# Optimization experiments

Measured on AMD Instinct MI355X. Metric: run time of the kernel, lower is better.

## Reference

```python
import jax, jax.numpy as jnp
import numpy as np

N, ID, OD, M, S, L = 65536, 16, 8, 1024, 8, 64


def setup_inputs() -> dict:
    key = jax.random.key(0)
    k1, k2, k3, k4, k5, k6 = jax.random.split(key, 6)
    return {
        "x": jax.random.normal(k1, (N, ID), dtype=jnp.float32),
        "inducing_locations": jax.random.uniform(k2, (M, ID), dtype=jnp.float32),
        "inducing_weights": jax.random.normal(k3, (S, OD, M), dtype=jnp.float32),
        "prior_frequency": jax.random.normal(k4, (OD, ID, L), dtype=jnp.float32),
        "prior_phase": jax.random.uniform(k5, (OD, L), dtype=jnp.float32, maxval=2 * np.pi),
        "prior_weights": jax.random.normal(k6, (S, OD, L), dtype=jnp.float32),
    }


def _rbf_matrix(x, z):
    # ExponentiatedQuadratic with amplitude=1, length_scale=1:
    # k(x,z) = exp(-0.5 * ||x - z||^2)
    x2 = jnp.sum(x * x, axis=-1)[:, None]          # [N,1]
    z2 = jnp.sum(z * z, axis=-1)[None, :]          # [1,M]
    sq = jnp.maximum(x2 + z2 - 2.0 * (x @ z.T), 0.0)
    return jnp.exp(-0.5 * sq)                      # [N,M]


def reference(x, inducing_locations, inducing_weights, prior_frequency, prior_phase, prior_weights):
    # ---- prior (random Fourier features) ----
    # spectral_weights for unit RBF: outer_weights = ones((OD,L)), inner_weights = ones((ID,))
    # rescaled_x = x / 1 = x
    # basis_fn_inner_prod: [OD, N, L]
    inner = jnp.einsum('ni,oil->onl', x, prior_frequency)
    basis_fn = jnp.cos(inner + prior_phase[:, None, :])              # [OD,N,L]
    basis_weight = jnp.sqrt(2.0 / prior_frequency.shape[-1]) * prior_weights  # [S,OD,L]
    f_prior = jnp.einsum('onl,sol->son', basis_fn, basis_weight)     # [S,OD,N]

    # ---- data term (kernel matrix + matvec) ----
    K = _rbf_matrix(x, inducing_locations)                           # [N,M]
    f_data = jnp.einsum('nm,som->son', K, inducing_weights)          # [S,OD,N]

    return f_prior + f_data
```

## Files before the change

kernel.cpp:

```cpp
#include <hip/hip_runtime.h>
#include <hip/hip_bf16.h>

#define N_PTS 65536
#define LOG2E 1.4426950408889634f
#define INV2PI 0.15915494309189535f

typedef __attribute__((ext_vector_type(8))) short short8;
typedef __attribute__((ext_vector_type(4))) short short4v;
typedef __attribute__((ext_vector_type(4))) float float4v;
typedef __attribute__((ext_vector_type(4))) unsigned int uint4v;

#if __has_builtin(__builtin_amdgcn_exp2f)
#define EXP2F(x) __builtin_amdgcn_exp2f(x)
#else
#define EXP2F(x) exp2f(x)
#endif

#if __has_builtin(__builtin_amdgcn_cosf) && __has_builtin(__builtin_amdgcn_fractf)
#define COSR(x) __builtin_amdgcn_cosf(__builtin_amdgcn_fractf(x))
#else
#define COSR(x) __cosf((x) * 6.283185307179586f)
#endif

__device__ __forceinline__ short f2b(float f) {
    __hip_bfloat16 h = __float2bfloat16(f);
    return *(short*)&h;
}
__device__ __forceinline__ float b2f(short s) {
    __hip_bfloat16 h = *(__hip_bfloat16*)&s;
    return __bfloat162float(h);
}

__device__ __forceinline__ unsigned int pkbf(float a, float b) {
    unsigned int ua = __builtin_bit_cast(unsigned int, a) + 0x8000u;
    unsigned int ub = __builtin_bit_cast(unsigned int, b) + 0x8000u;
    return (ua >> 16) | (ub & 0xFFFF0000u);
}

#if __has_builtin(__builtin_amdgcn_mfma_f32_16x16x16bf16_1k)
#define HAVE_MFMA16 1
typedef short4v pafrag;
__device__ __forceinline__ float4v pmfma(pafrag a, pafrag b, float4v c) {
    return __builtin_amdgcn_mfma_f32_16x16x16bf16_1k(a, b, c, 0, 0, 0);
}
#else
#define HAVE_MFMA16 0
typedef short8 pafrag;
__device__ __forceinline__ float4v pmfma(pafrag a, pafrag b, float4v c) {
    return __builtin_amdgcn_mfma_f32_16x16x32_bf16(a, b, c, 0, 0, 0);
}
#endif

__device__ __forceinline__ pafrag ldrow(const short* base, int row16, int q, int c) {
#if HAVE_MFMA16
    return *(const pafrag*)(base + (size_t)(row16 + c) * 16 + 4 * q);
#else
    pafrag v = (pafrag)0;
    if (q < 2) v = *(const pafrag*)(base + (size_t)(row16 + c) * 16 + 8 * q);
    return v;
#endif
}
__device__ __forceinline__ pafrag mkxfrag(const float* x, size_t row, int q) {
#if HAVE_MFMA16
    float4v v = *(const float4v*)(x + row * 16 + 4 * q);
    pafrag a;
    a[0] = f2b(v.x); a[1] = f2b(v.y); a[2] = f2b(v.z); a[3] = f2b(v.w);
    return a;
#else
    pafrag a = (pafrag)0;
    if (q < 2) {
        const float4v* xp = (const float4v*)(x + row * 16 + 8 * q);
        float4v v0 = xp[0], v1 = xp[1];
        a[0] = f2b(v0.x); a[1] = f2b(v0.y); a[2] = f2b(v0.z); a[3] = f2b(v0.w);
        a[4] = f2b(v1.x); a[5] = f2b(v1.y); a[6] = f2b(v1.z); a[7] = f2b(v1.w);
    }
    return a;
#endif
}

__device__ __forceinline__ int permrow(int p) {
    return ((p & 12) << 1) + (p & 3) + ((p >> 4) << 2);
}

__global__ __launch_bounds__(256) void prep_kernel(
    const float* __restrict__ z, const float* __restrict__ W,
    const float* __restrict__ F, const float* __restrict__ pw,
    const float* __restrict__ ph,
    short* __restrict__ zb, short* __restrict__ FbB,
    short* __restrict__ BWd, short* __restrict__ Wtb,
    float* __restrict__ nz2P, float* __restrict__ phP)
{
    int t = blockIdx.x * 256 + threadIdx.x;
    if (t < 16384) {
        int row = t >> 4, i = t & 15;
        int src = (row & ~31) + permrow(row & 31);
        zb[t] = f2b(LOG2E * z[src * 16 + i]);
    } else if (t < 17408) {
        int m = t - 16384;
        int src = (m & ~31) + permrow(m & 31);
        const float4v* zp = (const float4v*)(z + (size_t)src * 16);
        float s = 0.f;
        #pragma unroll
        for (int k = 0; k < 4; k++) {
            float4v v = zp[k];
            float a0 = b2f(f2b(v.x)), a1 = b2f(f2b(v.y));
            float a2 = b2f(f2b(v.z)), a3 = b2f(f2b(v.w));
            s += a0 * a0 + a1 * a1 + a2 * a2 + a3 * a3;
        }
        nz2P[m] = -(0.5f * LOG2E * s);
    } else if (t < 25600) {
        int p = t - 17408;
        int row = p >> 4, i = p & 15;
        int srow = (row & ~31) + permrow(row & 31);
        int o = srow >> 6, l = srow & 63;
        FbB[p] = f2b(INV2PI * F[o * 1024 + i * 64 + l]);
    } else if (t < 58368) {
        int p = t - 25600;
        int so = p >> 9, ol = p & 511, o = ol >> 6;
        float v = ((so & 7) == o) ? 0.17677669529663687f * pw[so * 64 + (ol & 63)] : 0.f;
        BWd[p] = f2b(v);
    } else if (t < 123904) {
        int p = t - 58368;
        Wtb[p] = f2b(W[p]);
    } else {
        int j = t - 123904;
        int sj = (j & ~31) + permrow(j & 31);
        phP[j] = INV2PI * ph[sj];
    }
}

__global__ __launch_bounds__(256, 4) void fused_kernel(
    const float* __restrict__ x,
    const short* __restrict__ zb, const short* __restrict__ FbB,
    const short* __restrict__ BWd, const short* __restrict__ Wtb,
    const float* __restrict__ nz2P, const float* __restrict__ phP,
    float* __restrict__ out)
{
    __shared__ float x2c[64];
    __shared__ __align__(16) float rbufA[64 * 68];
    __shared__ __align__(16) float rbufB[64 * 68];

    const int tid = threadIdx.x;
    const int lane = tid & 63, w = tid >> 6;
    const int q = lane >> 4, c = lane & 15;
    const int n0 = blockIdx.x * 64;

    if (tid < 64) {
        float s = 0.f;
        const float4v* xr = (const float4v*)(x + (size_t)(n0 + tid) * 16);
        #pragma unroll
        for (int k = 0; k < 4; k++) {
            float4v v = xr[k];
            float a0 = b2f(f2b(v.x)), a1 = b2f(f2b(v.y));
            float a2 = b2f(f2b(v.z)), a3 = b2f(f2b(v.w));
            s += a0 * a0 + a1 * a1 + a2 * a2 + a3 * a3;
        }
        x2c[tid] = 0.5f * LOG2E * s;
    }

    pafrag ax[4];
    #pragma unroll
    for (int nt = 0; nt < 4; nt++)
        ax[nt] = mkxfrag(x, (size_t)(n0 + nt * 16 + c), q);

    float4v acc[4][4];
    #pragma unroll
    for (int a = 0; a < 4; a++)
        #pragma unroll
        for (int nt = 0; nt < 4; nt++) acc[a][nt] = (float4v)(0.f);

    __syncthreads();

    const int mbase = w * 256;
    #pragma unroll 2
    for (int mb = 0; mb < 8; mb++) {
        const int m0 = mbase + mb * 32;
        pafrag bzA = ldrow(zb, m0, q, c);
        pafrag bzB = ldrow(zb, m0 + 16, q, c);
        float4v c0A = *(const float4v*)(nz2P + m0 + 4 * q);
        float4v c0B = *(const float4v*)(nz2P + m0 + 16 + 4 * q);
        short8 aw0 = *(const short8*)(Wtb + (size_t)(0 * 16 + c) * 1024 + m0 + q * 8);
        short8 aw1 = *(const short8*)(Wtb + (size_t)(1 * 16 + c) * 1024 + m0 + q * 8);
        short8 aw2 = *(const short8*)(Wtb + (size_t)(2 * 16 + c) * 1024 + m0 + q * 8);
        short8 aw3 = *(const short8*)(Wtb + (size_t)(3 * 16 + c) * 1024 + m0 + q * 8);
        #pragma unroll
        for (int nt = 0; nt < 4; nt++) {
            float4v dA = pmfma(bzA, ax[nt], c0A);
            float4v dB = pmfma(bzB, ax[nt], c0B);
            uint4v u;
            u[0] = pkbf(EXP2F(dA[0]), EXP2F(dA[1]));
            u[1] = pkbf(EXP2F(dA[2]), EXP2F(dA[3]));
            u[2] = pkbf(EXP2F(dB[0]), EXP2F(dB[1]));
            u[3] = pkbf(EXP2F(dB[2]), EXP2F(dB[3]));
            short8 pb = __builtin_bit_cast(short8, u);
            acc[0][nt] = __builtin_amdgcn_mfma_f32_16x16x32_bf16(aw0, pb, acc[0][nt], 0, 0, 0);
            acc[1][nt] = __builtin_amdgcn_mfma_f32_16x16x32_bf16(aw1, pb, acc[1][nt], 0, 0, 0);
            acc[2][nt] = __builtin_amdgcn_mfma_f32_16x16x32_bf16(aw2, pb, acc[2][nt], 0, 0, 0);
            acc[3][nt] = __builtin_amdgcn_mfma_f32_16x16x32_bf16(aw3, pb, acc[3][nt], 0, 0, 0);
        }
    }

    #pragma unroll
    for (int nt = 0; nt < 4; nt++) {
        float sxv = EXP2F(-x2c[nt * 16 + c]);
        #pragma unroll
        for (int a = 0; a < 4; a++) acc[a][nt] *= sxv;
    }

    const int lbase = w * 128;
    #pragma unroll 2
    for (int lb = 0; lb < 4; lb++) {
        const int l0 = lbase + lb * 32;
        pafrag bfA = ldrow(FbB, l0, q, c);
        pafrag bfB = ldrow(FbB, l0 + 16, q, c);
        float4v c0A = *(const float4v*)(phP + l0 + 4 * q);
        float4v c0B = *(const float4v*)(phP + l0 + 16 + 4 * q);
        short8 aw0 = *(const short8*)(BWd + (size_t)(0 * 16 + c) * 512 + l0 + q * 8);
        short8 aw1 = *(const short8*)(BWd + (size_t)(1 * 16 + c) * 512 + l0 + q * 8);
        short8 aw2 = *(const short8*)(BWd + (size_t)(2 * 16 + c) * 512 + l0 + q * 8);
        short8 aw3 = *(const short8*)(BWd + (size_t)(3 * 16 + c) * 512 + l0 + q * 8);
        #pragma unroll
        for (int nt = 0; nt < 4; nt++) {
            float4v dA = pmfma(bfA, ax[nt], c0A);
            float4v dB = pmfma(bfB, ax[nt], c0B);
            uint4v u;
            u[0] = pkbf(COSR(dA[0]), COSR(dA[1]));
            u[1] = pkbf(COSR(dA[2]), COSR(dA[3]));
            u[2] = pkbf(COSR(dB[0]), COSR(dB[1]));
            u[3] = pkbf(COSR(dB[2]), COSR(dB[3]));
            short8 pb = __builtin_bit_cast(short8, u);
            acc[0][nt] = __builtin_amdgcn_mfma_f32_16x16x32_bf16(aw0, pb, acc[0][nt], 0, 0, 0);
            acc[1][nt] = __builtin_amdgcn_mfma_f32_16x16x32_bf16(aw1, pb, acc[1][nt], 0, 0, 0);
            acc[2][nt] = __builtin_amdgcn_mfma_f32_16x16x32_bf16(aw2, pb, acc[2][nt], 0, 0, 0);
            acc[3][nt] = __builtin_amdgcn_mfma_f32_16x16x32_bf16(aw3, pb, acc[3][nt], 0, 0, 0);
        }
    }

    __syncthreads();
    if (w & 1) {
        float* rb = (w == 1) ? rbufA : rbufB;
        #pragma unroll
        for (int a = 0; a < 4; a++)
            #pragma unroll
            for (int nt = 0; nt < 4; nt++)
                #pragma unroll
                for (int r = 0; r < 4; r++)
                    rb[(a * 16 + 4 * q + r) * 68 + nt * 16 + c] = acc[a][nt][r];
    }
    __syncthreads();
    if (!(w & 1)) {
        float* rb = (w == 0) ? rbufA : rbufB;
        #pragma unroll
        for (int a = 0; a < 4; a++)
            #pragma unroll
            for (int nt = 0; nt < 4; nt++)
                #pragma unroll
                for (int r = 0; r < 4; r++) {
                    int idx = (a * 16 + 4 * q + r) * 68 + nt * 16 + c;
                    rb[idx] += acc[a][nt][r];
                }
    }
    __syncthreads();
    #pragma unroll
    for (int k = 0; k < 16; k++) {
        int idx = k * 256 + tid;
        int row = idx >> 6, nn = idx & 63;
        out[(size_t)row * N_PTS + n0 + nn] = rbufA[row * 68 + nn] + rbufB[row * 68 + nn];
    }
}

extern "C" void kernel_launch(void* const* d_in, const int* in_sizes, int n_in,
                              void* d_out, int out_size, void* d_ws, size_t ws_size,
                              hipStream_t stream) {
    const float* x  = (const float*)d_in[0];
    const float* z  = (const float*)d_in[1];
    const float* W  = (const float*)d_in[2];
    const float* F  = (const float*)d_in[3];
    const float* ph = (const float*)d_in[4];
    const float* pw = (const float*)d_in[5];
    float* out = (float*)d_out;

    char* ws = (char*)d_ws;
    short* zb   = (short*)(ws);
    short* FbB  = (short*)(ws + 32768);
    short* BWd  = (short*)(ws + 49152);
    short* Wtb  = (short*)(ws + 114688);
    float* nz2P = (float*)(ws + 245760);
    float* phP  = (float*)(ws + 249856);

    prep_kernel<<<486, 256, 0, stream>>>(z, W, F, pw, ph, zb, FbB, BWd, Wtb, nz2P, phP);
    fused_kernel<<<1024, 256, 0, stream>>>(x, zb, FbB, BWd, Wtb, nz2P, phP, out);
}
```

Measured before the change: 107.6 us.

## Fold parameter prep kernel into fused kernel, converting to bf16 on the fly

Removes the separate prep kernel launch and workspace. The fused kernel now reads the fp32 inducing locations, weights, frequencies and prior weights directly and converts them to bf16 fragments inside the main loops. The per-inducing-point norms and the phases are computed per block into shared memory that reuses the reduction buffer. This trades one launch and a small global round trip for redundant conversion work and twice the fp32 global/L2 read traffic in every one of 1024 blocks, plus strided loads for the frequency fragments.

```diff
diff --git a/kernel.cpp b/kernel.cpp
--- a/kernel.cpp
+++ b/kernel.cpp
@@ -4,11 +4,13 @@
 #define N_PTS 65536
 #define LOG2E 1.4426950408889634f
 #define INV2PI 0.15915494309189535f
+#define PWSC 0.17677669529663687f
 
 typedef __attribute__((ext_vector_type(8))) short short8;
 typedef __attribute__((ext_vector_type(4))) short short4v;
 typedef __attribute__((ext_vector_type(4))) float float4v;
 typedef __attribute__((ext_vector_type(4))) unsigned int uint4v;
+typedef __attribute__((ext_vector_type(2))) unsigned int uint2v;
 
 #if __has_builtin(__builtin_amdgcn_exp2f)
 #define EXP2F(x) __builtin_amdgcn_exp2f(x)
@@ -51,15 +53,79 @@
 }
 #endif
 
-__device__ __forceinline__ pafrag ldrow(const short* base, int row16, int q, int c) {
+__device__ __forceinline__ int permrow(int p) {
+    return ((p & 12) << 1) + (p & 3) + ((p >> 4) << 2);
+}
+
+
+__device__ __forceinline__ pafrag mkzfrag(const float* __restrict__ z, int p, int q) {
+    int src = (p & ~31) + permrow(p & 31);
 #if HAVE_MFMA16
-    return *(const pafrag*)(base + (size_t)(row16 + c) * 16 + 4 * q);
-#else
-    pafrag v = (pafrag)0;
-    if (q < 2) v = *(const pafrag*)(base + (size_t)(row16 + c) * 16 + 8 * q);
-    return v;
-#endif
-}
+    float4v v = *(const float4v*)(z + (size_t)src * 16 + 4 * q);
+    uint2v u;
+    u[0] = pkbf(LOG2E * v.x, LOG2E * v.y);
+    u[1] = pkbf(LOG2E * v.z, LOG2E * v.w);
+    return __builtin_bit_cast(short4v, u);
+#else
+    pafrag a = (pafrag)0;
+    if (q < 2) {
+        const float4v* zp = (const float4v*)(z + (size_t)src * 16 + 8 * q);
+        float4v v0 = zp[0], v1 = zp[1];
+        uint4v u;
+        u[0] = pkbf(LOG2E * v0.x, LOG2E * v0.y);
+        u[1] = pkbf(LOG2E * v0.z, LOG2E * v0.w);
+        u[2] = pkbf(LOG2E * v1.x, LOG2E * v1.y);
+        u[3] = pkbf(LOG2E * v1.z, LOG2E * v1.w);
+        a = __builtin_bit_cast(short8, u);
+    }
+    return a;
+#endif
+}
+
+__device__ __forceinline__ pafrag mkffrag(const float* __restrict__ F, int p, int q) {
+    int srow = (p & ~31) + permrow(p & 31);
+    const float* fb = F + ((srow >> 6) << 10) + (srow & 63);
+#if HAVE_MFMA16
+    float d0 = fb[(4 * q + 0) * 64], d1 = fb[(4 * q + 1) * 64];
+    float d2 = fb[(4 * q + 2) * 64], d3 = fb[(4 * q + 3) * 64];
+    uint2v u;
+    u[0] = pkbf(INV2PI * d0, INV2PI * d1);
+    u[1] = pkbf(INV2PI * d2, INV2PI * d3);
+    return __builtin_bit_cast(short4v, u);
+#else
+    pafrag a = (pafrag)0;
+    if (q < 2) {
+        uint4v u;
+        #pragma unroll
+        for (int j = 0; j < 4; j++) {
+            float g0 = fb[(8 * q + 2 * j) * 64], g1 = fb[(8 * q + 2 * j + 1) * 64];
+            u[j] = pkbf(INV2PI * g0, INV2PI * g1);
+        }
+        a = __builtin_bit_cast(short8, u);
+    }
+    return a;
+#endif
+}
+
+__device__ __forceinline__ short8 mkwfrag(const float* __restrict__ W, int so, int base) {
+    const float4v* wp = (const float4v*)(W + (size_t)so * 1024 + base);
+    float4v v0 = wp[0], v1 = wp[1];
+    uint4v u;
+    u[0] = pkbf(v0.x, v0.y); u[1] = pkbf(v0.z, v0.w);
+    u[2] = pkbf(v1.x, v1.y); u[3] = pkbf(v1.z, v1.w);
+    return __builtin_bit_cast(short8, u);
+}
+
+__device__ __forceinline__ short8 mkbwfrag(const float* __restrict__ pw, int so, int base) {
+    float s = ((so & 7) == (base >> 6)) ? PWSC : 0.f;
+    const float4v* pp = (const float4v*)(pw + (size_t)so * 64 + (base & 63));
+    float4v v0 = pp[0], v1 = pp[1];
+    uint4v u;
+    u[0] = pkbf(s * v0.x, s * v0.y); u[1] = pkbf(s * v0.z, s * v0.w);
+    u[2] = pkbf(s * v1.x, s * v1.y); u[3] = pkbf(s * v1.z, s * v1.w);
+    return __builtin_bit_cast(short8, u);
+}
+
 __device__ __forceinline__ pafrag mkxfrag(const float* x, size_t row, int q) {
 #if HAVE_MFMA16
     float4v v = *(const float4v*)(x + row * 16 + 4 * q);
@@ -78,73 +144,44 @@
 #endif
 }
 
-__device__ __forceinline__ int permrow(int p) {
-    return ((p & 12) << 1) + (p & 3) + ((p >> 4) << 2);
-}
-
-__global__ __launch_bounds__(256) void prep_kernel(
-    const float* __restrict__ z, const float* __restrict__ W,
-    const float* __restrict__ F, const float* __restrict__ pw,
-    const float* __restrict__ ph,
-    short* __restrict__ zb, short* __restrict__ FbB,
-    short* __restrict__ BWd, short* __restrict__ Wtb,
-    float* __restrict__ nz2P, float* __restrict__ phP)
-{
-    int t = blockIdx.x * 256 + threadIdx.x;
-    if (t < 16384) {
-        int row = t >> 4, i = t & 15;
-        int src = (row & ~31) + permrow(row & 31);
-        zb[t] = f2b(LOG2E * z[src * 16 + i]);
-    } else if (t < 17408) {
-        int m = t - 16384;
-        int src = (m & ~31) + permrow(m & 31);
-        const float4v* zp = (const float4v*)(z + (size_t)src * 16);
-        float s = 0.f;
-        #pragma unroll
-        for (int k = 0; k < 4; k++) {
-            float4v v = zp[k];
-            float a0 = b2f(f2b(v.x)), a1 = b2f(f2b(v.y));
-            float a2 = b2f(f2b(v.z)), a3 = b2f(f2b(v.w));
-            s += a0 * a0 + a1 * a1 + a2 * a2 + a3 * a3;
-        }
-        nz2P[m] = -(0.5f * LOG2E * s);
-    } else if (t < 25600) {
-        int p = t - 17408;
-        int row = p >> 4, i = p & 15;
-        int srow = (row & ~31) + permrow(row & 31);
-        int o = srow >> 6, l = srow & 63;
-        FbB[p] = f2b(INV2PI * F[o * 1024 + i * 64 + l]);
-    } else if (t < 58368) {
-        int p = t - 25600;
-        int so = p >> 9, ol = p & 511, o = ol >> 6;
-        float v = ((so & 7) == o) ? 0.17677669529663687f * pw[so * 64 + (ol & 63)] : 0.f;
-        BWd[p] = f2b(v);
-    } else if (t < 123904) {
-        int p = t - 58368;
-        Wtb[p] = f2b(W[p]);
-    } else {
-        int j = t - 123904;
-        int sj = (j & ~31) + permrow(j & 31);
-        phP[j] = INV2PI * ph[sj];
-    }
-}
-
 __global__ __launch_bounds__(256, 4) void fused_kernel(
-    const float* __restrict__ x,
-    const short* __restrict__ zb, const short* __restrict__ FbB,
-    const short* __restrict__ BWd, const short* __restrict__ Wtb,
-    const float* __restrict__ nz2P, const float* __restrict__ phP,
+    const float* __restrict__ x, const float* __restrict__ z,
+    const float* __restrict__ W, const float* __restrict__ F,
+    const float* __restrict__ ph, const float* __restrict__ pw,
     float* __restrict__ out)
 {
     __shared__ float x2c[64];
     __shared__ __align__(16) float rbufA[64 * 68];
     __shared__ __align__(16) float rbufB[64 * 68];
+    float* nz2L = rbufA;
+    float* phL  = rbufA + 1024;
 
     const int tid = threadIdx.x;
     const int lane = tid & 63, w = tid >> 6;
     const int q = lane >> 4, c = lane & 15;
     const int n0 = blockIdx.x * 64;
 
+    #pragma unroll
+    for (int k = 0; k < 4; k++) {
+        int m = tid + k * 256;
+        int src = (m & ~31) + permrow(m & 31);
+        const float4v* zp = (const float4v*)(z + (size_t)src * 16);
+        float s = 0.f;
+        #pragma unroll
+        for (int kk = 0; kk < 4; kk++) {
+            float4v v = zp[kk];
+            float a0 = b2f(f2b(v.x)), a1 = b2f(f2b(v.y));
+            float a2 = b2f(f2b(v.z)), a3 = b2f(f2b(v.w));
+            s += a0 * a0 + a1 * a1 + a2 * a2 + a3 * a3;
+        }
+        nz2L[m] = -(0.5f * LOG2E * s);
+    }
+    #pragma unroll
+    for (int k = 0; k < 2; k++) {
+        int j = tid + k * 256;
+        int sj = (j & ~31) + permrow(j & 31);
+        phL[j] = INV2PI * ph[sj];
+    }
     if (tid < 64) {
         float s = 0.f;
         const float4v* xr = (const float4v*)(x + (size_t)(n0 + tid) * 16);
@@ -175,14 +212,14 @@
     #pragma unroll 2
     for (int mb = 0; mb < 8; mb++) {
         const int m0 = mbase + mb * 32;
-        pafrag bzA = ldrow(zb, m0, q, c);
-        pafrag bzB = ldrow(zb, m0 + 16, q, c);
-        float4v c0A = *(const float4v*)(nz2P + m0 + 4 * q);
-        float4v c0B = *(const float4v*)(nz2P + m0 + 16 + 4 * q);
-        short8 aw0 = *(const short8*)(Wtb + (size_t)(0 * 16 + c) * 1024 + m0 + q * 8);
-        short8 aw1 = *(const short8*)(Wtb + (size_t)(1 * 16 + c) * 1024 + m0 + q * 8);
-        short8 aw2 = *(const short8*)(Wtb + (size_t)(2 * 16 + c) * 1024 + m0 + q * 8);
-        short8 aw3 = *(const short8*)(Wtb + (size_t)(3 * 16 + c) * 1024 + m0 + q * 8);
+        pafrag bzA = mkzfrag(z, m0 + c, q);
+        pafrag bzB = mkzfrag(z, m0 + 16 + c, q);
+        float4v c0A = *(const float4v*)(nz2L + m0 + 4 * q);
+        float4v c0B = *(const float4v*)(nz2L + m0 + 16 + 4 * q);
+        short8 aw0 = mkwfrag(W, 0 * 16 + c, m0 + q * 8);
+        short8 aw1 = mkwfrag(W, 1 * 16 + c, m0 + q * 8);
+        short8 aw2 = mkwfrag(W, 2 * 16 + c, m0 + q * 8);
+        short8 aw3 = mkwfrag(W, 3 * 16 + c, m0 + q * 8);
         #pragma unroll
         for (int nt = 0; nt < 4; nt++) {
             float4v dA = pmfma(bzA, ax[nt], c0A);
@@ -211,14 +248,14 @@
     #pragma unroll 2
     for (int lb = 0; lb < 4; lb++) {
         const int l0 = lbase + lb * 32;
-        pafrag bfA = ldrow(FbB, l0, q, c);
-        pafrag bfB = ldrow(FbB, l0 + 16, q, c);
-        float4v c0A = *(const float4v*)(phP + l0 + 4 * q);
-        float4v c0B = *(const float4v*)(phP + l0 + 16 + 4 * q);
-        short8 aw0 = *(const short8*)(BWd + (size_t)(0 * 16 + c) * 512 + l0 + q * 8);
-        short8 aw1 = *(const short8*)(BWd + (size_t)(1 * 16 + c) * 512 + l0 + q * 8);
-        short8 aw2 = *(const short8*)(BWd + (size_t)(2 * 16 + c) * 512 + l0 + q * 8);
-        short8 aw3 = *(const short8*)(BWd + (size_t)(3 * 16 + c) * 512 + l0 + q * 8);
+        pafrag bfA = mkffrag(F, l0 + c, q);
+        pafrag bfB = mkffrag(F, l0 + 16 + c, q);
+        float4v c0A = *(const float4v*)(phL + l0 + 4 * q);
+        float4v c0B = *(const float4v*)(phL + l0 + 16 + 4 * q);
+        short8 aw0 = mkbwfrag(pw, 0 * 16 + c, l0 + q * 8);
+        short8 aw1 = mkbwfrag(pw, 1 * 16 + c, l0 + q * 8);
+        short8 aw2 = mkbwfrag(pw, 2 * 16 + c, l0 + q * 8);
+        short8 aw3 = mkbwfrag(pw, 3 * 16 + c, l0 + q * 8);
         #pragma unroll
         for (int nt = 0; nt < 4; nt++) {
             float4v dA = pmfma(bfA, ax[nt], c0A);
@@ -280,14 +317,6 @@
     const float* pw = (const float*)d_in[5];
     float* out = (float*)d_out;
 
-    char* ws = (char*)d_ws;
-    short* zb   = (short*)(ws);
-    short* FbB  = (short*)(ws + 32768);
-    short* BWd  = (short*)(ws + 49152);
-    short* Wtb  = (short*)(ws + 114688);
-    float* nz2P = (float*)(ws + 245760);
-    float* phP  = (float*)(ws + 249856);
-
-    prep_kernel<<<486, 256, 0, stream>>>(z, W, F, pw, ph, zb, FbB, BWd, Wtb, nz2P, phP);
-    fused_kernel<<<1024, 256, 0, stream>>>(x, zb, FbB, BWd, Wtb, nz2P, phP, out);
-}
+    (void)d_ws; (void)ws_size;
+    fused_kernel<<<1024, 256, 0, stream>>>(x, z, W, F, ph, pw, out);
+}
```

Result: slower. 160.4 us (+49.1%).
